# Optimization experiments

Measured on AMD Instinct MI355X. Metric: run time of the kernel, lower is better.

Reference implementation:

```python
import jax, jax.numpy as jnp
import numpy as np

B, N, NFEAT = 8, 2048, 128
RED = NFEAT // 2          # 64
K_G = 8                   # hard-coded ksize in LUMLP -> DSgroupMLP
K_LU = 16                 # k for FeatureLaplacian
EPS = 1e-5                # BatchNorm eps (torch default)


def _bn_relu(y, g, b):
    # BatchNorm1d in training mode: biased batch stats over (batch, spatial)
    mu = y.mean(axis=(0, 2), keepdims=True)
    var = y.var(axis=(0, 2), keepdims=True)
    return jax.nn.relu((y - mu) * jax.lax.rsqrt(var + EPS) * g[None, :, None] + b[None, :, None])


def _cbr(x, W, b, g, bt):
    # ConvBNReLU1D with kernel_size=1: pointwise linear + BN + ReLU
    y = jnp.einsum('oc,bcn->bon', W, x) + b[None, :, None]
    return _bn_relu(y, g, bt)


def _bknn(x, k):
    # x: [B, C, N]; returns top-k nearest-neighbor indices [B, N, k]
    inner = 2.0 * jnp.einsum('bcn,bcm->bnm', x, x)
    xx = jnp.sum(x * x, axis=1)                         # [B, N]
    dist = xx[:, :, None] - inner + xx[:, None, :]      # [B, N, N]
    return jax.lax.top_k(-dist, k)[1]


def setup_inputs() -> dict:
    key = jax.random.key(0)
    ks = jax.random.split(key, 8)
    def w(k_, o, i):
        return jax.random.normal(k_, (o, i), jnp.float32) / np.sqrt(i)
    return {
        'xyz': jax.random.normal(ks[0], (B, 3, N), jnp.float32),
        'feat': jax.random.normal(ks[1], (B, NFEAT, N), jnp.float32),
        # mlp1: nfeat -> redfeat
        'w1': w(ks[2], RED, NFEAT), 'b1': jnp.zeros((RED,), jnp.float32),
        'g1': jnp.ones((RED,), jnp.float32), 'be1': jnp.zeros((RED,), jnp.float32),
        # DSgroupMLP fc1 + bn1
        'wf': w(ks[3], RED, RED), 'bf': jnp.zeros((RED,), jnp.float32),
        'gg': jnp.ones((RED,), jnp.float32), 'bg': jnp.zeros((RED,), jnp.float32),
        # FeatureLaplacian transform + batchNorm
        'wl': w(ks[4], RED, RED), 'bl': jnp.zeros((RED,), jnp.float32),
        'gl': jnp.ones((RED,), jnp.float32), 'bel': jnp.zeros((RED,), jnp.float32),
        # mlp2: redfeat -> nfeat
        'w2': w(ks[5], NFEAT, RED), 'b2': jnp.zeros((NFEAT,), jnp.float32),
        'g2': jnp.ones((NFEAT,), jnp.float32), 'be2': jnp.zeros((NFEAT,), jnp.float32),
        # mlp3: nfeat -> 2*nfeat
        'w3': w(ks[6], 2 * NFEAT, NFEAT), 'b3': jnp.zeros((2 * NFEAT,), jnp.float32),
        'g3': jnp.ones((2 * NFEAT,), jnp.float32), 'be3': jnp.zeros((2 * NFEAT,), jnp.float32),
    }


def reference(xyz, feat, w1, b1, g1, be1, wf, bf, gg, bg, wl, bl, gl, bel,
              w2, b2, g2, be2, w3, b3, g3, be3):
    # ---- mlp1 ----
    x = _cbr(feat, w1, b1, g1, be1)                      # [B, RED, N]
    Bm, Fm, Nm = x.shape
    # ---- DSgroupMLP (ksize = 8) ----
    idx = _bknn(xyz[:, :2, :], K_G)                      # [B, N, K]
    def gather_g(fb, ib):
        # faithful torch .view: [F, N*K] -> [F, K, N]
        return fb[:, ib.reshape(-1)].reshape(Fm, K_G, Nm)
    grp = jax.vmap(gather_g)(x, idx)                     # [B, F, K, N]
    gq = grp.transpose(0, 3, 2, 1)                       # [B, N, K, F]
    h = jnp.einsum('bnkf,of->bnko', gq, wf) + bf         # fc1 over F
    h = h.reshape(Bm, Nm * K_G, Fm).transpose(0, 2, 1)   # [B, F, N*K]
    h = _bn_relu(h, gg, bg)
    x = h.reshape(Bm, Fm, Nm, K_G).max(axis=-1)          # max-pool over K
    # ---- FeatureLaplacian (k = 16) ----
    idx2 = _bknn(xyz[:, :2, :], K_LU)                    # [B, N, k]
    def lapfn(fb, ib):
        # faithful torch .view: [F, N*k] -> [N, k, F]
        lf = fb[:, ib.reshape(-1)].reshape(Nm, K_LU, Fm)
        return fb.T - lf.mean(axis=1)                    # [N, F]
    lap = jax.vmap(lapfn)(x, idx2)                       # [B, N, F]
    t = jnp.einsum('bnf,of->bon', lap, wl) + bl[None, :, None]  # [B, F, N]
    t = _bn_relu(t, gl, bel)
    x = x + t
    # ---- mlp2 + residual + mlp3 ----
    y = _cbr(x, w2, b2, g2, be2) + feat                  # [B, NFEAT, N]
    return _cbr(y, w3, b3, g3, be3)                      # [B, 2*NFEAT, N]
```

## Files before the change

kernel.cpp:

```cpp
#include <hip/hip_runtime.h>

#define NB   8
#define NPT  2048
#define NF   128
#define CR   64
#define EPSI 1e-5

__global__ void __launch_bounds__(256) knn_kernel(const float* __restrict__ xyz,
                                                  int* __restrict__ idx16) {
  __shared__ float px[NPT], py[NPT], sxx[NPT];
  int b = blockIdx.x >> 9;
  const float* xb = xyz + b * 3 * NPT;
  for (int i = threadIdx.x; i < NPT; i += 256) {
    float x = xb[i], y = xb[NPT + i];
    px[i] = x; py[i] = y;
    sxx[i] = __fadd_rn(__fmul_rn(x, x), __fmul_rn(y, y));
  }
  __syncthreads();
  int lane = threadIdx.x & 63, wid = threadIdx.x >> 6;
  int q = ((blockIdx.x & 511) << 2) | wid;
  float qx = px[q], qy = py[q], qxx = sxx[q];
  float dc[32];
#pragma unroll 4
  for (int j = 0; j < 32; ++j) {
    int m = lane + (j << 6);
    float inner_s = __fmaf_rn(qy, py[m], __fmul_rn(qx, px[m]));
    dc[j] = __fadd_rn(__fsub_rn(qxx, __fmul_rn(2.0f, inner_s)), sxx[m]);
  }
  int keep = 0;
  for (int r = 0; r < 16; ++r) {
    float dmin = dc[0]; int jmin = 0;
#pragma unroll
    for (int j = 1; j < 32; ++j) {
      bool better = dc[j] < dmin;
      dmin = better ? dc[j] : dmin;
      jmin = better ? j : jmin;
    }
    float hd = dmin;
    int   hm = lane + (jmin << 6);
#pragma unroll
    for (int off = 1; off < 64; off <<= 1) {
      float od = __shfl_xor(hd, off);
      int   om = __shfl_xor(hm, off);
      bool take = (od < hd) || (od == hd && om < hm);
      hd = take ? od : hd;
      hm = take ? om : hm;
    }
    if (lane == r) keep = hm;
    bool own = (hm & 63) == lane;
    int jw = hm >> 6;
#pragma unroll
    for (int j = 0; j < 32; ++j)
      dc[j] = (own && j == jw) ? 1e38f : dc[j];
  }
  if (lane < 16) idx16[((b * NPT + q) << 4) + lane] = keep;
}

template<int IC, int OC>
__global__ void __launch_bounds__(256) conv_stats(const float* __restrict__ in,
                                                  const float* __restrict__ w,
                                                  const float* __restrict__ bias,
                                                  float* __restrict__ outp,
                                                  double* __restrict__ stats) {
  int bz = blockIdx.x;
  int n  = ((bz & 7) << 8) | threadIdx.x;
  int o0 = ((bz >> 3) % (OC / 8)) * 8;
  int b  = bz / (8 * (OC / 8));
  const float* inb = in + b * IC * NPT + n;
  float a[8];
#pragma unroll
  for (int t = 0; t < 8; ++t) a[t] = bias[o0 + t];
  const float* wb = w + o0 * IC;
#pragma unroll 4
  for (int f = 0; f < IC; ++f) {
    float v = inb[f * NPT];
#pragma unroll
    for (int t = 0; t < 8; ++t) a[t] += wb[t * IC + f] * v;
  }
  float* ob = outp + b * OC * NPT + n;
#pragma unroll
  for (int t = 0; t < 8; ++t) ob[(o0 + t) * NPT] = a[t];
  __shared__ double red[4][8][2];
  int lane = threadIdx.x & 63, wid = threadIdx.x >> 6;
#pragma unroll
  for (int j = 0; j < 8; ++j) {
    double s1 = (double)a[j];
    double s2 = (double)a[j] * (double)a[j];
#pragma unroll
    for (int off = 32; off; off >>= 1) { s1 += __shfl_down(s1, off); s2 += __shfl_down(s2, off); }
    if (lane == 0) { red[wid][j][0] = s1; red[wid][j][1] = s2; }
  }
  __syncthreads();
  if (threadIdx.x < 8) {
    int j = threadIdx.x;
    double S1 = red[0][j][0] + red[1][j][0] + red[2][j][0] + red[3][j][0];
    double S2 = red[0][j][1] + red[1][j][1] + red[2][j][1] + red[3][j][1];
    atomicAdd(&stats[o0 + j], S1);
    atomicAdd(&stats[OC + o0 + j], S2);
  }
}

template<int C>
__global__ void __launch_bounds__(256) bn_apply(const float* __restrict__ pre,
                                                const float* __restrict__ addsrc,
                                                float* __restrict__ outp,
                                                const double* __restrict__ stats,
                                                const float* __restrict__ gam,
                                                const float* __restrict__ bet,
                                                double inv_cnt) {
  __shared__ float sc[C], sh[C];
  for (int c = threadIdx.x; c < C; c += 256) {
    double mu    = stats[c] * inv_cnt;
    double var   = stats[C + c] * inv_cnt - mu * mu;
    double scale = (double)gam[c] / sqrt(var + EPSI);
    sc[c] = (float)scale;
    sh[c] = (float)((double)bet[c] - mu * scale);
  }
  __syncthreads();
  const float4* pre4 = (const float4*)pre;
  const float4* add4 = (const float4*)addsrc;
  float4* out4 = (float4*)outp;
  int total4 = NB * C * (NPT / 4);
  for (int i = blockIdx.x * 256 + threadIdx.x; i < total4; i += gridDim.x * 256) {
    int c = (i >> 9) & (C - 1);
    float s = sc[c], h = sh[c];
    float4 v = pre4[i];
    v.x = fmaxf(v.x * s + h, 0.f);
    v.y = fmaxf(v.y * s + h, 0.f);
    v.z = fmaxf(v.z * s + h, 0.f);
    v.w = fmaxf(v.w * s + h, 0.f);
    if (addsrc) {
      float4 a = add4[i];
      v.x += a.x; v.y += a.y; v.z += a.z; v.w += a.w;
    }
    out4[i] = v;
  }
}

__global__ void __launch_bounds__(256) dsgroup_kernel(const float* __restrict__ x1,
                                                      const int* __restrict__ idx16,
                                                      const float* __restrict__ wf,
                                                      const float* __restrict__ bfp,
                                                      float* __restrict__ hmax,
                                                      double* __restrict__ stats) {
  __shared__ float wfT[64 * 65];
  __shared__ double dred[4][64][2];
  for (int i = threadIdx.x; i < 64 * 64; i += 256) {
    int o = i >> 6, f = i & 63;
    wfT[f * 65 + o] = wf[i];
  }
  __syncthreads();
  int lane = threadIdx.x & 63, wid = threadIdx.x >> 6;
  int wave = blockIdx.x * 4 + wid;
  float bo = bfp[lane];
  double s1 = 0.0, s2 = 0.0;
  for (int p = 0; p < 4; ++p) {
    int pt = wave * 4 + p;
    int b = pt >> 11, n = pt & 2047;
    int src[8];
#pragma unroll
    for (int k = 0; k < 8; ++k) {
      int j = k * NPT + n;
      src[k] = idx16[((b * NPT + (j >> 3)) << 4) | (j & 7)];
    }
    float acc[8];
#pragma unroll
    for (int k = 0; k < 8; ++k) acc[k] = bo;
    const float* x1b = x1 + b * CR * NPT;
    for (int f = 0; f < 64; ++f) {
      float wv = wfT[f * 65 + lane];
      const float* row = x1b + f * NPT;
#pragma unroll
      for (int k = 0; k < 8; ++k) acc[k] += row[src[k]] * wv;
    }
    float hm = acc[0];
#pragma unroll
    for (int k = 0; k < 8; ++k) {
      hm = fmaxf(hm, acc[k]);
      s1 += (double)acc[k];
      s2 += (double)acc[k] * (double)acc[k];
    }
    hmax[(b * CR + lane) * NPT + n] = hm;
  }
  dred[wid][lane][0] = s1; dred[wid][lane][1] = s2;
  __syncthreads();
  if (threadIdx.x < 64) {
    double S1 = dred[0][threadIdx.x][0] + dred[1][threadIdx.x][0] + dred[2][threadIdx.x][0] + dred[3][threadIdx.x][0];
    double S2 = dred[0][threadIdx.x][1] + dred[1][threadIdx.x][1] + dred[2][threadIdx.x][1] + dred[3][threadIdx.x][1];
    atomicAdd(&stats[threadIdx.x], S1);
    atomicAdd(&stats[64 + threadIdx.x], S2);
  }
}

__global__ void __launch_bounds__(256) lap_fused(const float* __restrict__ hpre,
                                                 const int* __restrict__ idx16,
                                                 const float* __restrict__ wl,
                                                 const float* __restrict__ blp,
                                                 float* __restrict__ tpre,
                                                 double* __restrict__ stats,
                                                 const double* __restrict__ stg,
                                                 const float* __restrict__ gg,
                                                 const float* __restrict__ bg) {
  __shared__ float wlT[64 * 65];
  __shared__ double dred[4][64][2];
  __shared__ float vstage[4][64];
  __shared__ float scg[64], shg[64];
  for (int i = threadIdx.x; i < 64 * 64; i += 256) {
    int o = i >> 6, f = i & 63;
    wlT[f * 65 + o] = wl[i];
  }
  if (threadIdx.x < 64) {
    int c = threadIdx.x;
    double mu  = stg[c] / 131072.0;
    double var = stg[64 + c] / 131072.0 - mu * mu;
    double s   = (double)gg[c] / sqrt(var + EPSI);
    scg[c] = (float)s;
    shg[c] = (float)((double)bg[c] - mu * s);
  }
  __syncthreads();
  int lane = threadIdx.x & 63, wid = threadIdx.x >> 6;
  int g = lane >> 4, cc = lane & 15;
  float blv = blp[lane];
  double s1 = 0.0, s2 = 0.0;
  for (int p = 0; p < 4; ++p) {
    int pt = (blockIdx.x * 4 + wid) * 4 + p;
    int b = pt >> 11, n = pt & 2047;
    int ch = n >> 5;
    int r0 = (n & 31) << 6;
    const float* xrow = hpre + (b * CR + ch) * NPT;
    const int* ib = idx16 + ((b * NPT + r0) << 4);
    float sgc = scg[ch], shc = shg[ch];
    float msum = 0.f;
#pragma unroll
    for (int kk = 0; kk < 16; ++kk) {
      int sidx = ib[(((kk << 2) + g) << 4) | cc];
      msum += fmaxf(fmaf(xrow[sidx], sgc, shc), 0.f);
    }
    float mval = msum * 0.0625f;
    float xraw = hpre[(b * CR + lane) * NPT + n];
    float xv = fmaxf(fmaf(xraw, scg[lane], shg[lane]), 0.f);
    vstage[wid][lane] = xv - mval;
    float acc = blv;
    for (int f = 0; f < 64; ++f)
      acc += wlT[f * 65 + lane] * vstage[wid][f];
    tpre[(b * CR + lane) * NPT + n] = acc;
    s1 += (double)acc;
    s2 += (double)acc * (double)acc;
  }
  dred[wid][lane][0] = s1; dred[wid][lane][1] = s2;
  __syncthreads();
  if (threadIdx.x < 64) {
    double S1 = dred[0][threadIdx.x][0] + dred[1][threadIdx.x][0] + dred[2][threadIdx.x][0] + dred[3][threadIdx.x][0];
    double S2 = dred[0][threadIdx.x][1] + dred[1][threadIdx.x][1] + dred[2][threadIdx.x][1] + dred[3][threadIdx.x][1];
    atomicAdd(&stats[threadIdx.x], S1);
    atomicAdd(&stats[64 + threadIdx.x], S2);
  }
}

__global__ void __launch_bounds__(256) combine_kernel(float* __restrict__ hpre,
                                                      const float* __restrict__ tpre,
                                                      const double* __restrict__ stg,
                                                      const float* __restrict__ gg,
                                                      const float* __restrict__ bg,
                                                      const double* __restrict__ stl,
                                                      const float* __restrict__ gl,
                                                      const float* __restrict__ bel) {
  __shared__ float scg[64], shg[64], scl[64], shl[64];
  if (threadIdx.x < 64) {
    int c = threadIdx.x;
    double mu  = stg[c] / 131072.0;
    double var = stg[64 + c] / 131072.0 - mu * mu;
    double s   = (double)gg[c] / sqrt(var + EPSI);
    scg[c] = (float)s; shg[c] = (float)((double)bg[c] - mu * s);
    double mu2  = stl[c] / 16384.0;
    double var2 = stl[64 + c] / 16384.0 - mu2 * mu2;
    double s2   = (double)gl[c] / sqrt(var2 + EPSI);
    scl[c] = (float)s2; shl[c] = (float)((double)bel[c] - mu2 * s2);
  }
  __syncthreads();
  float4* h4 = (float4*)hpre;
  const float4* t4 = (const float4*)tpre;
  int total4 = NB * CR * (NPT / 4);
  for (int i = blockIdx.x * 256 + threadIdx.x; i < total4; i += gridDim.x * 256) {
    int c = (i >> 9) & 63;
    float sg = scg[c], hg = shg[c], sl = scl[c], hl = shl[c];
    float4 h = h4[i];
    float4 t = t4[i];
    h.x = fmaxf(h.x * sg + hg, 0.f) + fmaxf(t.x * sl + hl, 0.f);
    h.y = fmaxf(h.y * sg + hg, 0.f) + fmaxf(t.y * sl + hl, 0.f);
    h.z = fmaxf(h.z * sg + hg, 0.f) + fmaxf(t.z * sl + hl, 0.f);
    h.w = fmaxf(h.w * sg + hg, 0.f) + fmaxf(t.w * sl + hl, 0.f);
    h4[i] = h;
  }
}

extern "C" void kernel_launch(void* const* d_in, const int* in_sizes, int n_in,
                              void* d_out, int out_size, void* d_ws, size_t ws_size,
                              hipStream_t stream) {
  const float* xyz  = (const float*)d_in[0];
  const float* feat = (const float*)d_in[1];
  const float* w1   = (const float*)d_in[2];
  const float* b1   = (const float*)d_in[3];
  const float* g1   = (const float*)d_in[4];
  const float* be1  = (const float*)d_in[5];
  const float* wf   = (const float*)d_in[6];
  const float* bf   = (const float*)d_in[7];
  const float* gg   = (const float*)d_in[8];
  const float* bg   = (const float*)d_in[9];
  const float* wl   = (const float*)d_in[10];
  const float* bl   = (const float*)d_in[11];
  const float* gl   = (const float*)d_in[12];
  const float* bel  = (const float*)d_in[13];
  const float* w2   = (const float*)d_in[14];
  const float* b2   = (const float*)d_in[15];
  const float* g2   = (const float*)d_in[16];
  const float* be2  = (const float*)d_in[17];
  const float* w3   = (const float*)d_in[18];
  const float* b3   = (const float*)d_in[19];
  const float* g3   = (const float*)d_in[20];
  const float* be3  = (const float*)d_in[21];
  float* out = (float*)d_out;

  float* x1   = out;
  float* tpre = out + 1048576;
  int*  idx16 = (int*)(out + 2097152);
  float*  hpre  = (float*)d_ws;
  float*  y2    = hpre + 1048576;
  double* stats = (double*)((char*)d_ws + (12u << 20));
  double* st0 = stats;
  double* stg = stats + 128;
  double* stl = stats + 256;
  double* st2 = stats + 384;
  double* st3 = stats + 640;

  hipMemsetAsync(stats, 0, 1152 * sizeof(double), stream);

  knn_kernel<<<4096, 256, 0, stream>>>(xyz, idx16);
  conv_stats<128, 64><<<512, 256, 0, stream>>>(feat, w1, b1, x1, st0);
  bn_apply<64><<<1024, 256, 0, stream>>>(x1, nullptr, x1, st0, g1, be1, 1.0 / 16384.0);
  dsgroup_kernel<<<1024, 256, 0, stream>>>(x1, idx16, wf, bf, hpre, stg);
  lap_fused<<<1024, 256, 0, stream>>>(hpre, idx16, wl, bl, tpre, stl, stg, gg, bg);
  combine_kernel<<<1024, 256, 0, stream>>>(hpre, tpre, stg, gg, bg, stl, gl, bel);
  conv_stats<64, 128><<<1024, 256, 0, stream>>>(hpre, w2, b2, y2, st2);
  bn_apply<128><<<1024, 256, 0, stream>>>(y2, feat, y2, st2, g2, be2, 1.0 / 16384.0);
  conv_stats<128, 256><<<2048, 256, 0, stream>>>(y2, w3, b3, out, st3);
  bn_apply<256><<<1024, 256, 0, stream>>>(out, nullptr, out, st3, g3, be3, 1.0 / 16384.0);
}
```

Measured before the change: 301.0 us.

## Fuse combine into mlp2 conv, widen mlp3 conv tile, scalarize group indices

Folds the BN+ReLU combine of the group and Laplacian branches into the loads of the mlp2 pointwise conv, so the combined tensor is no longer written and re-read. Adds a 16-output-channel variant of the conv+stats kernel for mlp3, halving the grid and reusing each input load across more outputs at the cost of more registers. Marks the gathered neighbor indices in the group kernel as wave-uniform via readfirstlane so they go through scalar loads. The fused conv recomputes the BN transform for each output-channel block, and that duplicated work is part of the trade.

Result: no change. 306.2 us (+1.7%).

```diff
diff --git a/kernel.cpp b/kernel.cpp
--- a/kernel.cpp
+++ b/kernel.cpp
@@ -92,6 +92,50 @@
   }
   __syncthreads();
   if (threadIdx.x < 8) {
+    int j = threadIdx.x;
+    double S1 = red[0][j][0] + red[1][j][0] + red[2][j][0] + red[3][j][0];
+    double S2 = red[0][j][1] + red[1][j][1] + red[2][j][1] + red[3][j][1];
+    atomicAdd(&stats[o0 + j], S1);
+    atomicAdd(&stats[OC + o0 + j], S2);
+  }
+}
+
+template<int IC, int OC>
+__global__ void __launch_bounds__(256) conv_stats16(const float* __restrict__ in,
+                                                    const float* __restrict__ w,
+                                                    const float* __restrict__ bias,
+                                                    float* __restrict__ outp,
+                                                    double* __restrict__ stats) {
+  int bz = blockIdx.x;
+  int n  = ((bz & 7) << 8) | threadIdx.x;
+  int o0 = ((bz >> 3) % (OC / 16)) * 16;
+  int b  = bz / (8 * (OC / 16));
+  const float* inb = in + b * IC * NPT + n;
+  float a[16];
+#pragma unroll
+  for (int t = 0; t < 16; ++t) a[t] = bias[o0 + t];
+  const float* wb = w + o0 * IC;
+#pragma unroll 2
+  for (int f = 0; f < IC; ++f) {
+    float v = inb[f * NPT];
+#pragma unroll
+    for (int t = 0; t < 16; ++t) a[t] += wb[t * IC + f] * v;
+  }
+  float* ob = outp + b * OC * NPT + n;
+#pragma unroll
+  for (int t = 0; t < 16; ++t) ob[(o0 + t) * NPT] = a[t];
+  __shared__ double red[4][16][2];
+  int lane = threadIdx.x & 63, wid = threadIdx.x >> 6;
+#pragma unroll
+  for (int j = 0; j < 16; ++j) {
+    double s1 = (double)a[j];
+    double s2 = (double)a[j] * (double)a[j];
+#pragma unroll
+    for (int off = 32; off; off >>= 1) { s1 += __shfl_down(s1, off); s2 += __shfl_down(s2, off); }
+    if (lane == 0) { red[wid][j][0] = s1; red[wid][j][1] = s2; }
+  }
+  __syncthreads();
+  if (threadIdx.x < 16) {
     int j = threadIdx.x;
     double S1 = red[0][j][0] + red[1][j][0] + red[2][j][0] + red[3][j][0];
     double S2 = red[0][j][1] + red[1][j][1] + red[2][j][1] + red[3][j][1];
@@ -161,7 +205,7 @@
 #pragma unroll
     for (int k = 0; k < 8; ++k) {
       int j = k * NPT + n;
-      src[k] = idx16[((b * NPT + (j >> 3)) << 4) | (j & 7)];
+      src[k] = __builtin_amdgcn_readfirstlane(idx16[((b * NPT + (j >> 3)) << 4) | (j & 7)]);
     }
     float acc[8];
 #pragma unroll
@@ -257,15 +301,20 @@
   }
 }
 
-__global__ void __launch_bounds__(256) combine_kernel(float* __restrict__ hpre,
-                                                      const float* __restrict__ tpre,
-                                                      const double* __restrict__ stg,
-                                                      const float* __restrict__ gg,
-                                                      const float* __restrict__ bg,
-                                                      const double* __restrict__ stl,
-                                                      const float* __restrict__ gl,
-                                                      const float* __restrict__ bel) {
+__global__ void __launch_bounds__(256) conv2_fused(const float* __restrict__ hpre,
+                                                   const float* __restrict__ tpre,
+                                                   const double* __restrict__ stg,
+                                                   const float* __restrict__ gg,
+                                                   const float* __restrict__ bg,
+                                                   const double* __restrict__ stl,
+                                                   const float* __restrict__ gl,
+                                                   const float* __restrict__ bel,
+                                                   const float* __restrict__ w,
+                                                   const float* __restrict__ bias,
+                                                   float* __restrict__ outp,
+                                                   double* __restrict__ stats) {
   __shared__ float scg[64], shg[64], scl[64], shl[64];
+  __shared__ double red[4][8][2];
   if (threadIdx.x < 64) {
     int c = threadIdx.x;
     double mu  = stg[c] / 131072.0;
@@ -278,19 +327,42 @@
     scl[c] = (float)s2; shl[c] = (float)((double)bel[c] - mu2 * s2);
   }
   __syncthreads();
-  float4* h4 = (float4*)hpre;
-  const float4* t4 = (const float4*)tpre;
-  int total4 = NB * CR * (NPT / 4);
-  for (int i = blockIdx.x * 256 + threadIdx.x; i < total4; i += gridDim.x * 256) {
-    int c = (i >> 9) & 63;
-    float sg = scg[c], hg = shg[c], sl = scl[c], hl = shl[c];
-    float4 h = h4[i];
-    float4 t = t4[i];
-    h.x = fmaxf(h.x * sg + hg, 0.f) + fmaxf(t.x * sl + hl, 0.f);
-    h.y = fmaxf(h.y * sg + hg, 0.f) + fmaxf(t.y * sl + hl, 0.f);
-    h.z = fmaxf(h.z * sg + hg, 0.f) + fmaxf(t.z * sl + hl, 0.f);
-    h.w = fmaxf(h.w * sg + hg, 0.f) + fmaxf(t.w * sl + hl, 0.f);
-    h4[i] = h;
+  int bz = blockIdx.x;
+  int n  = ((bz & 7) << 8) | threadIdx.x;
+  int o0 = ((bz >> 3) % 16) * 8;
+  int b  = bz / 128;
+  const float* hb = hpre + b * CR * NPT + n;
+  const float* tb = tpre + b * CR * NPT + n;
+  float a[8];
+#pragma unroll
+  for (int t = 0; t < 8; ++t) a[t] = bias[o0 + t];
+  const float* wb = w + o0 * CR;
+#pragma unroll 4
+  for (int f = 0; f < CR; ++f) {
+    float hv = hb[f * NPT], tv = tb[f * NPT];
+    float v = fmaxf(fmaf(hv, scg[f], shg[f]), 0.f) + fmaxf(fmaf(tv, scl[f], shl[f]), 0.f);
+#pragma unroll
+    for (int t = 0; t < 8; ++t) a[t] += wb[t * CR + f] * v;
+  }
+  float* ob = outp + b * NF * NPT + n;
+#pragma unroll
+  for (int t = 0; t < 8; ++t) ob[(o0 + t) * NPT] = a[t];
+  int lane = threadIdx.x & 63, wid = threadIdx.x >> 6;
+#pragma unroll
+  for (int j = 0; j < 8; ++j) {
+    double s1 = (double)a[j];
+    double s2 = (double)a[j] * (double)a[j];
+#pragma unroll
+    for (int off = 32; off; off >>= 1) { s1 += __shfl_down(s1, off); s2 += __shfl_down(s2, off); }
+    if (lane == 0) { red[wid][j][0] = s1; red[wid][j][1] = s2; }
+  }
+  __syncthreads();
+  if (threadIdx.x < 8) {
+    int j = threadIdx.x;
+    double S1 = red[0][j][0] + red[1][j][0] + red[2][j][0] + red[3][j][0];
+    double S2 = red[0][j][1] + red[1][j][1] + red[2][j][1] + red[3][j][1];
+    atomicAdd(&stats[o0 + j], S1);
+    atomicAdd(&stats[NF + o0 + j], S2);
   }
 }
 
@@ -340,9 +412,8 @@
   bn_apply<64><<<1024, 256, 0, stream>>>(x1, nullptr, x1, st0, g1, be1, 1.0 / 16384.0);
   dsgroup_kernel<<<1024, 256, 0, stream>>>(x1, idx16, wf, bf, hpre, stg);
   lap_fused<<<1024, 256, 0, stream>>>(hpre, idx16, wl, bl, tpre, stl, stg, gg, bg);
-  combine_kernel<<<1024, 256, 0, stream>>>(hpre, tpre, stg, gg, bg, stl, gl, bel);
-  conv_stats<64, 128><<<1024, 256, 0, stream>>>(hpre, w2, b2, y2, st2);
+  conv2_fused<<<1024, 256, 0, stream>>>(hpre, tpre, stg, gg, bg, stl, gl, bel, w2, b2, y2, st2);
   bn_apply<128><<<1024, 256, 0, stream>>>(y2, feat, y2, st2, g2, be2, 1.0 / 16384.0);
-  conv_stats<128, 256><<<2048, 256, 0, stream>>>(y2, w3, b3, out, st3);
+  conv_stats16<128, 256><<<1024, 256, 0, stream>>>(y2, w3, b3, out, st3);
   bn_apply<256><<<1024, 256, 0, stream>>>(out, nullptr, out, st3, g3, be3, 1.0 / 16384.0);
 }
```
